# Kernel tuning notes

Hardware: AMD Instinct MI355X
Metric: run time of the kernel (lower is better)

The kernel has to match this reference:

```python
import jax, jax.numpy as jnp
import numpy as np

H = 3072           # hidden_size
I = 8192           # intermediate_size
GS = 128           # quantization group size
B, S = 2, 2048


def dequant(qw, qz, scales, group_size=GS):
    """Group-wise int4 dequant: w = (q - zero) * scale.
    qw: [out, in] int8 nibbles in [0,16); qz: [out, in//g] int8; scales: [out, in//g] f32.
    """
    zp = jnp.repeat(qz.astype(jnp.float32), group_size, axis=1)
    sc = jnp.repeat(scales, group_size, axis=1)
    return (qw.astype(jnp.float32) - zp) * sc


def setup_inputs() -> dict:
    key = jax.random.key(0)
    ks = jax.random.split(key, 8)
    hidden_states = jax.random.normal(ks[0], (B, S, H), dtype=jnp.float32)
    # gate_up projection: [2*I, H], group-quantized along the input (H) dim
    gup_qw = jax.random.randint(ks[1], (2 * I, H), 0, 16, dtype=jnp.int8)
    gup_qz = jax.random.randint(ks[2], (2 * I, H // GS), 0, 16, dtype=jnp.int8)
    gup_scales = jax.random.uniform(ks[3], (2 * I, H // GS), dtype=jnp.float32, minval=0.005, maxval=0.02)
    # down projection: [H, I], group-quantized along the input (I) dim
    down_qw = jax.random.randint(ks[4], (H, I), 0, 16, dtype=jnp.int8)
    down_qz = jax.random.randint(ks[5], (H, I // GS), 0, 16, dtype=jnp.int8)
    down_scales = jax.random.uniform(ks[6], (H, I // GS), dtype=jnp.float32, minval=0.005, maxval=0.02)
    down_bias = jnp.zeros((H,), dtype=jnp.float32)
    return {
        "hidden_states": hidden_states,
        "gup_qw": gup_qw, "gup_qz": gup_qz, "gup_scales": gup_scales,
        "down_qw": down_qw, "down_qz": down_qz, "down_scales": down_scales,
        "down_bias": down_bias,
    }


def reference(hidden_states, gup_qw, gup_qz, gup_scales, down_qw, down_qz, down_scales, down_bias):
    W_gup = dequant(gup_qw, gup_qz, gup_scales)           # [2I, H]
    up_states = jnp.einsum('bsh,oh->bso', hidden_states, W_gup)  # [B,S,2I]
    gate, up = jnp.split(up_states, 2, axis=-1)
    act = jax.nn.silu(gate) * up                          # fused gate*act*up
    W_down = dequant(down_qw, down_qz, down_scales)       # [H, I]
    out = jnp.einsum('bsi,hi->bsh', act, W_down) + down_bias
    return out
```

## Files before the change

kernel.cpp:

```cpp
#include <hip/hip_runtime.h>


typedef float f32x4 __attribute__((ext_vector_type(4)));
typedef int   i32x4 __attribute__((ext_vector_type(4)));

__device__ __forceinline__ void gload16(const void* g, void* l) {
  __builtin_amdgcn_global_load_lds(
      (const __attribute__((address_space(1))) void*)g,
      (__attribute__((address_space(3))) void*)l, 16, 0, 0);
}

__global__ __launch_bounds__(256) void quant_x(const float* __restrict__ x,
                                               signed char* __restrict__ Xq,
                                               float* __restrict__ XsT) {
  int gidx = blockIdx.x * 4 + (threadIdx.x >> 6);
  int lane = threadIdx.x & 63;
  int row = gidx / 24;
  int g   = gidx - row * 24;
  const float2 v = *(const float2*)(x + (size_t)row * 3072 + g * 128 + lane * 2);
  float m = fmaxf(fabsf(v.x), fabsf(v.y));
#pragma unroll
  for (int s = 1; s < 64; s <<= 1) m = fmaxf(m, __shfl_xor(m, s));
  float inv = m > 0.f ? 127.f / m : 0.f;
  int qa = (int)rintf(v.x * inv);
  int qb = (int)rintf(v.y * inv);
  unsigned short pk = (unsigned short)((qa & 0xff) | ((qb & 0xff) << 8));
  *(unsigned short*)(Xq + (size_t)row * 3072 + g * 128 + lane * 2) = pk;
  if (lane == 0) XsT[g * 4096 + row] = m * (1.f / 127.f);
}

template <int K>
__global__ __launch_bounds__(256) void requant_k(const int* __restrict__ qw,
                                                 const int* __restrict__ qz,
                                                 signed char* __restrict__ W) {
  constexpr int KG = K / 128;
  constexpr int perrow = K / 8;
  int idx = blockIdx.x * 256 + threadIdx.x;
  int row = idx / perrow;
  int c8  = idx - row * perrow;
  int k   = c8 << 3;
  int z   = qz[row * KG + (k >> 7)];
  const int4* q4 = (const int4*)(qw + (size_t)row * K + k);
  int4 qa = q4[0];
  int4 qb = q4[1];
  int b0 = ((qa.x - z) & 0xff) | (((qa.y - z) & 0xff) << 8) |
           (((qa.z - z) & 0xff) << 16) | (((qa.w - z) & 0xff) << 24);
  int b1 = ((qb.x - z) & 0xff) | (((qb.y - z) & 0xff) << 8) |
           (((qb.z - z) & 0xff) << 16) | (((qb.w - z) & 0xff) << 24);
  int2 o; o.x = b0; o.y = b1;
  *(int2*)(W + (size_t)row * K + k) = o;
}

__global__ __launch_bounds__(256) void transpose_sc(const float* __restrict__ in,
                                                    float* __restrict__ out,
                                                    int R, int G) {
  int idx = blockIdx.x * 256 + threadIdx.x;
  int r = idx / G;
  int g = idx - r * G;
  out[(size_t)g * R + r] = in[idx];
}


__global__ __launch_bounds__(256, 2) void gemm_gateup_i8(
    const signed char* __restrict__ Xq, const signed char* __restrict__ Wq,
    const float* __restrict__ XsT,
    const float* __restrict__ GsT,
    signed char* __restrict__ act,
    float* __restrict__ AsT) {
  const int K = 3072;
  const int bid = blockIdx.x;
  const int xcd = bid & 7;
  const int jb  = bid >> 3;
  const int n0  = ((xcd << 3) + (jb & 7)) * 128;
  const int m0  = (jb >> 3) * 128;
  __shared__ signed char lA[16384];
  __shared__ signed char lG[16384];
  __shared__ signed char lU[16384];
  __shared__ float rmax[2][128];

  const int tid  = threadIdx.x;
  const int l    = tid & 63;
  const int quad = l >> 4;
  const int l16  = l & 15;
  const int wcI  = (tid >> 6) & 1;
  const int wr   = ((tid >> 6) >> 1) * 64;
  const int wc   = wcI * 64;

  f32x4 fg[4][4] = {};
  f32x4 fu[4][4] = {};

  int off[4];
#pragma unroll
  for (int jj = 0; jj < 4; ++jj) {
    int c   = tid + 256 * jj;
    int row = c >> 3;
    int log = (c & 7) ^ (row & 7);
    off[jj] = row * K + log * 16;
  }
  const signed char* baseA = Xq + (size_t)m0 * K;
  const signed char* baseG = Wq + (size_t)n0 * K;
  const signed char* baseU = Wq + (size_t)(8192 + n0) * K;

  int aoff[2][4], boff[2][4];
#pragma unroll
  for (int h = 0; h < 2; ++h) {
    int slot = h * 4 + quad;
#pragma unroll
    for (int i = 0; i < 4; ++i) {
      int ra = wr + i * 16 + l16;
      aoff[h][i] = ra * 128 + ((slot ^ (ra & 7)) * 16);
      int rb = wc + i * 16 + l16;
      boff[h][i] = rb * 128 + ((slot ^ (rb & 7)) * 16);
    }
  }

  for (int g = 0; g < 24; ++g) {
    const int kk = g << 7;
#pragma unroll
    for (int jj = 0; jj < 4; ++jj) {
      gload16(baseA + off[jj] + kk, lA + (tid + 256 * jj) * 16);
      gload16(baseG + off[jj] + kk, lG + (tid + 256 * jj) * 16);
      gload16(baseU + off[jj] + kk, lU + (tid + 256 * jj) * 16);
    }
    f32x4 sx[4];
    float sg[4], su[4];
#pragma unroll
    for (int i = 0; i < 4; ++i)
      sx[i] = *(const f32x4*)(XsT + g * 4096 + m0 + wr + i * 16 + quad * 4);
#pragma unroll
    for (int jj = 0; jj < 4; ++jj) {
      sg[jj] = GsT[g * 16384 + n0 + wc + jj * 16 + l16];
      su[jj] = GsT[g * 16384 + 8192 + n0 + wc + jj * 16 + l16];
    }
    __syncthreads();

    i32x4 a[4][2];
#pragma unroll
    for (int i = 0; i < 4; ++i) {
      a[i][0] = *(const i32x4*)(lA + aoff[0][i]);
      a[i][1] = *(const i32x4*)(lA + aoff[1][i]);
    }
#pragma unroll
    for (int jj = 0; jj < 4; ++jj) {
      i32x4 bg0 = *(const i32x4*)(lG + boff[0][jj]);
      i32x4 bg1 = *(const i32x4*)(lG + boff[1][jj]);
      i32x4 bu0 = *(const i32x4*)(lU + boff[0][jj]);
      i32x4 bu1 = *(const i32x4*)(lU + boff[1][jj]);
#pragma unroll
      for (int i = 0; i < 4; ++i) {
        i32x4 zero = {0, 0, 0, 0};
        i32x4 ig = __builtin_amdgcn_mfma_i32_16x16x64_i8(a[i][0], bg0, zero, 0, 0, 0);
        ig = __builtin_amdgcn_mfma_i32_16x16x64_i8(a[i][1], bg1, ig, 0, 0, 0);
        i32x4 iu = __builtin_amdgcn_mfma_i32_16x16x64_i8(a[i][0], bu0, zero, 0, 0, 0);
        iu = __builtin_amdgcn_mfma_i32_16x16x64_i8(a[i][1], bu1, iu, 0, 0, 0);
#pragma unroll
        for (int r = 0; r < 4; ++r) {
          float sc = sx[i][r];
          fg[i][jj][r] = fmaf((float)ig[r], sc * sg[jj], fg[i][jj][r]);
          fu[i][jj][r] = fmaf((float)iu[r], sc * su[jj], fu[i][jj][r]);
        }
      }
    }
    __syncthreads();
  }

#pragma unroll
  for (int i = 0; i < 4; ++i)
#pragma unroll
    for (int jj = 0; jj < 4; ++jj)
#pragma unroll
      for (int r = 0; r < 4; ++r) {
        float gv = fg[i][jj][r];
        float uv = fu[i][jj][r];
        fg[i][jj][r] = (gv / (1.f + __expf(-gv))) * uv;
      }

  float rmx[4][4];
#pragma unroll
  for (int i = 0; i < 4; ++i)
#pragma unroll
    for (int r = 0; r < 4; ++r) {
      float m = 0.f;
#pragma unroll
      for (int jj = 0; jj < 4; ++jj) m = fmaxf(m, fabsf(fg[i][jj][r]));
      m = fmaxf(m, __shfl_xor(m, 1));
      m = fmaxf(m, __shfl_xor(m, 2));
      m = fmaxf(m, __shfl_xor(m, 4));
      m = fmaxf(m, __shfl_xor(m, 8));
      rmx[i][r] = m;
    }
  if (l16 == 0) {
#pragma unroll
    for (int i = 0; i < 4; ++i)
#pragma unroll
      for (int r = 0; r < 4; ++r)
        rmax[wcI][wr + i * 16 + quad * 4 + r] = rmx[i][r];
  }
  __syncthreads();

#pragma unroll
  for (int i = 0; i < 4; ++i)
#pragma unroll
    for (int r = 0; r < 4; ++r) {
      int mrow = wr + i * 16 + quad * 4 + r;
      float mx = fmaxf(rmax[0][mrow], rmax[1][mrow]);
      float inv = mx > 0.f ? 127.f / mx : 0.f;
#pragma unroll
      for (int jj = 0; jj < 4; ++jj) {
        int q = (int)rintf(fg[i][jj][r] * inv);
        lA[mrow * 128 + wc + jj * 16 + l16] = (signed char)q;
      }
    }
  if (tid < 128) {
    float mx = fmaxf(rmax[0][tid], rmax[1][tid]);
    AsT[(n0 >> 7) * 4096 + m0 + tid] = mx * (1.f / 127.f);
  }
  __syncthreads();

#pragma unroll
  for (int t = 0; t < 4; ++t) {
    int c = tid + 256 * t;
    int row = c >> 3;
    int col = (c & 7) * 16;
    *(int4*)(act + (size_t)(m0 + row) * 8192 + n0 + col) = *(const int4*)(lA + row * 128 + col);
  }
}

__global__ __launch_bounds__(256, 2) void gemm_down_i8(
    const signed char* __restrict__ Aq, const signed char* __restrict__ Wq,
    const float* __restrict__ AsT,
    const float* __restrict__ DsT,
    const float* __restrict__ bias,
    float* __restrict__ out) {
  const int K = 8192;
  const int bid = blockIdx.x;
  const int xcd = bid & 7;
  const int jb  = bid >> 3;
  const int jn  = jb % 12;
  const int jm  = jb / 12;
  const int n0  = (12 * (xcd & 1) + jn) * 128;
  const int m0  = (8 * (xcd >> 1) + jm) * 128;
  __shared__ signed char lA[16384];
  __shared__ signed char lB[16384];

  const int tid  = threadIdx.x;
  const int l    = tid & 63;
  const int quad = l >> 4;
  const int l16  = l & 15;
  const int wr   = ((tid >> 6) >> 1) * 64;
  const int wc   = ((tid >> 6) & 1) * 64;

  f32x4 fc[4][4] = {};

  int off[4];
#pragma unroll
  for (int jj = 0; jj < 4; ++jj) {
    int c   = tid + 256 * jj;
    int row = c >> 3;
    int log = (c & 7) ^ (row & 7);
    off[jj] = row * K + log * 16;
  }
  const signed char* baseA = Aq + (size_t)m0 * K;
  const signed char* baseB = Wq + (size_t)n0 * K;

  int aoff[2][4], boff[2][4];
#pragma unroll
  for (int h = 0; h < 2; ++h) {
    int slot = h * 4 + quad;
#pragma unroll
    for (int i = 0; i < 4; ++i) {
      int ra = wr + i * 16 + l16;
      aoff[h][i] = ra * 128 + ((slot ^ (ra & 7)) * 16);
      int rb = wc + i * 16 + l16;
      boff[h][i] = rb * 128 + ((slot ^ (rb & 7)) * 16);
    }
  }

  for (int g = 0; g < 64; ++g) {
    const int kk = g << 7;
#pragma unroll
    for (int jj = 0; jj < 4; ++jj) {
      gload16(baseA + off[jj] + kk, lA + (tid + 256 * jj) * 16);
      gload16(baseB + off[jj] + kk, lB + (tid + 256 * jj) * 16);
    }
    f32x4 sx[4];
    float sn[4];
#pragma unroll
    for (int i = 0; i < 4; ++i)
      sx[i] = *(const f32x4*)(AsT + g * 4096 + m0 + wr + i * 16 + quad * 4);
#pragma unroll
    for (int jj = 0; jj < 4; ++jj)
      sn[jj] = DsT[g * 3072 + n0 + wc + jj * 16 + l16];
    __syncthreads();

    i32x4 a[4][2];
#pragma unroll
    for (int i = 0; i < 4; ++i) {
      a[i][0] = *(const i32x4*)(lA + aoff[0][i]);
      a[i][1] = *(const i32x4*)(lA + aoff[1][i]);
    }
#pragma unroll
    for (int jj = 0; jj < 4; ++jj) {
      i32x4 b0 = *(const i32x4*)(lB + boff[0][jj]);
      i32x4 b1 = *(const i32x4*)(lB + boff[1][jj]);
#pragma unroll
      for (int i = 0; i < 4; ++i) {
        i32x4 zero = {0, 0, 0, 0};
        i32x4 ic = __builtin_amdgcn_mfma_i32_16x16x64_i8(a[i][0], b0, zero, 0, 0, 0);
        ic = __builtin_amdgcn_mfma_i32_16x16x64_i8(a[i][1], b1, ic, 0, 0, 0);
#pragma unroll
        for (int r = 0; r < 4; ++r)
          fc[i][jj][r] = fmaf((float)ic[r], sx[i][r] * sn[jj], fc[i][jj][r]);
      }
    }
    __syncthreads();
  }

  float bj[4];
#pragma unroll
  for (int jj = 0; jj < 4; ++jj) bj[jj] = bias[n0 + wc + jj * 16 + l16];

#pragma unroll
  for (int i = 0; i < 4; ++i)
#pragma unroll
    for (int jj = 0; jj < 4; ++jj)
#pragma unroll
      for (int r = 0; r < 4; ++r) {
        int m = m0 + wr + i * 16 + quad * 4 + r;
        int n = n0 + wc + jj * 16 + l16;
        out[(size_t)m * 3072 + n] = fc[i][jj][r] + bj[jj];
      }
}

extern "C" void kernel_launch(void* const* d_in, const int* in_sizes, int n_in,
                              void* d_out, int out_size, void* d_ws, size_t ws_size,
                              hipStream_t stream) {
  const float* x        = (const float*)d_in[0];
  const int*   gup_qw   = (const int*)d_in[1];
  const int*   gup_qz   = (const int*)d_in[2];
  const float* gup_sc   = (const float*)d_in[3];
  const int*   down_qw  = (const int*)d_in[4];
  const int*   down_qz  = (const int*)d_in[5];
  const float* down_sc  = (const float*)d_in[6];
  const float* down_b   = (const float*)d_in[7];
  float* out = (float*)d_out;

  char* ws = (char*)d_ws;
  signed char* Xq    = (signed char*)(ws);
  signed char* Wgupq = (signed char*)(ws + 12582912);
  signed char* Wdnq  = (signed char*)(ws + 62914560);
  signed char* Actq  = (signed char*)(ws + 88080384);
  float* XsT = (float*)(ws + 121634816);
  float* GsT = (float*)(ws + 122028032);
  float* DsT = (float*)(ws + 123600896);
  float* AsT = (float*)(ws + 124387328);

  quant_x<<<24576, 256, 0, stream>>>(x, Xq, XsT);
  requant_k<3072><<<24576, 256, 0, stream>>>(gup_qw, gup_qz, Wgupq);
  requant_k<8192><<<12288, 256, 0, stream>>>(down_qw, down_qz, Wdnq);
  transpose_sc<<<1536, 256, 0, stream>>>(gup_sc, GsT, 16384, 24);
  transpose_sc<<<768, 256, 0, stream>>>(down_sc, DsT, 3072, 64);
  gemm_gateup_i8<<<2048, 256, 0, stream>>>(Xq, Wgupq, XsT, GsT, Actq, AsT);
  gemm_down_i8<<<768, 256, 0, stream>>>(Actq, Wdnq, AsT, DsT, down_b, out);
}
```

Before: 837.3 us.

## Share activation quant scales across 4-row groups and use packed f32x2 FMAs

Activation quantization scales for X and for the intermediate act are now shared by groups of 4 rows instead of one per row. Inside the GEMM loops each MFMA output vector then needs a single scale product, so the dequant-accumulate can use packed 2-wide FMAs. This is meant to cut VALU work and scale loads in the inner loop of both GEMMs. In exchange, quantization is coarser (one max over 4 rows), which raises quantization error for rows with smaller magnitudes.

```diff
diff --git a/kernel.cpp b/kernel.cpp
--- a/kernel.cpp
+++ b/kernel.cpp
@@ -2,6 +2,7 @@
 
 
 typedef float f32x4 __attribute__((ext_vector_type(4)));
+typedef float f32x2 __attribute__((ext_vector_type(2)));
 typedef int   i32x4 __attribute__((ext_vector_type(4)));
 
 __device__ __forceinline__ void gload16(const void* g, void* l) {
@@ -12,21 +13,26 @@
 
 __global__ __launch_bounds__(256) void quant_x(const float* __restrict__ x,
                                                signed char* __restrict__ Xq,
-                                               float* __restrict__ XsT) {
-  int gidx = blockIdx.x * 4 + (threadIdx.x >> 6);
+                                               float* __restrict__ Xs4) {
+  int g    = blockIdx.x;
+  int rq   = blockIdx.y;
+  int w    = threadIdx.x >> 6;
   int lane = threadIdx.x & 63;
-  int row = gidx / 24;
-  int g   = gidx - row * 24;
+  int row  = rq * 4 + w;
+  __shared__ float wmax[4];
   const float2 v = *(const float2*)(x + (size_t)row * 3072 + g * 128 + lane * 2);
   float m = fmaxf(fabsf(v.x), fabsf(v.y));
 #pragma unroll
   for (int s = 1; s < 64; s <<= 1) m = fmaxf(m, __shfl_xor(m, s));
-  float inv = m > 0.f ? 127.f / m : 0.f;
+  if (lane == 0) wmax[w] = m;
+  __syncthreads();
+  float m4 = fmaxf(fmaxf(wmax[0], wmax[1]), fmaxf(wmax[2], wmax[3]));
+  float inv = m4 > 0.f ? 127.f / m4 : 0.f;
   int qa = (int)rintf(v.x * inv);
   int qb = (int)rintf(v.y * inv);
   unsigned short pk = (unsigned short)((qa & 0xff) | ((qb & 0xff) << 8));
   *(unsigned short*)(Xq + (size_t)row * 3072 + g * 128 + lane * 2) = pk;
-  if (lane == 0) XsT[g * 4096 + row] = m * (1.f / 127.f);
+  if (threadIdx.x == 0) Xs4[g * 1024 + rq] = m4 * (1.f / 127.f);
 }
 
 template <int K>
@@ -63,10 +69,10 @@
 
 __global__ __launch_bounds__(256, 2) void gemm_gateup_i8(
     const signed char* __restrict__ Xq, const signed char* __restrict__ Wq,
-    const float* __restrict__ XsT,
+    const float* __restrict__ Xs4,
     const float* __restrict__ GsT,
     signed char* __restrict__ act,
-    float* __restrict__ AsT) {
+    float* __restrict__ As4) {
   const int K = 3072;
   const int bid = blockIdx.x;
   const int xcd = bid & 7;
@@ -77,6 +83,7 @@
   __shared__ signed char lG[16384];
   __shared__ signed char lU[16384];
   __shared__ float rmax[2][128];
+  __shared__ float rmax4[32];
 
   const int tid  = threadIdx.x;
   const int l    = tid & 63;
@@ -86,8 +93,8 @@
   const int wr   = ((tid >> 6) >> 1) * 64;
   const int wc   = wcI * 64;
 
-  f32x4 fg[4][4] = {};
-  f32x4 fu[4][4] = {};
+  f32x2 fg[4][4][2] = {};
+  f32x2 fu[4][4][2] = {};
 
   int off[4];
 #pragma unroll
@@ -113,6 +120,7 @@
       boff[h][i] = rb * 128 + ((slot ^ (rb & 7)) * 16);
     }
   }
+  const int qbase = (m0 >> 2) + (wr >> 2) + quad;
 
   for (int g = 0; g < 24; ++g) {
     const int kk = g << 7;
@@ -122,11 +130,9 @@
       gload16(baseG + off[jj] + kk, lG + (tid + 256 * jj) * 16);
       gload16(baseU + off[jj] + kk, lU + (tid + 256 * jj) * 16);
     }
-    f32x4 sx[4];
-    float sg[4], su[4];
-#pragma unroll
-    for (int i = 0; i < 4; ++i)
-      sx[i] = *(const f32x4*)(XsT + g * 4096 + m0 + wr + i * 16 + quad * 4);
+    float sxq[4], sg[4], su[4];
+#pragma unroll
+    for (int i = 0; i < 4; ++i) sxq[i] = Xs4[g * 1024 + qbase + i * 4];
 #pragma unroll
     for (int jj = 0; jj < 4; ++jj) {
       sg[jj] = GsT[g * 16384 + n0 + wc + jj * 16 + l16];
@@ -153,67 +159,72 @@
         ig = __builtin_amdgcn_mfma_i32_16x16x64_i8(a[i][1], bg1, ig, 0, 0, 0);
         i32x4 iu = __builtin_amdgcn_mfma_i32_16x16x64_i8(a[i][0], bu0, zero, 0, 0, 0);
         iu = __builtin_amdgcn_mfma_i32_16x16x64_i8(a[i][1], bu1, iu, 0, 0, 0);
-#pragma unroll
-        for (int r = 0; r < 4; ++r) {
-          float sc = sx[i][r];
-          fg[i][jj][r] = fmaf((float)ig[r], sc * sg[jj], fg[i][jj][r]);
-          fu[i][jj][r] = fmaf((float)iu[r], sc * su[jj], fu[i][jj][r]);
-        }
+        float pgs = sxq[i] * sg[jj];
+        float pus = sxq[i] * su[jj];
+        f32x2 pg2 = {pgs, pgs};
+        f32x2 pu2 = {pus, pus};
+        f32x2 g01 = {(float)ig[0], (float)ig[1]};
+        f32x2 g23 = {(float)ig[2], (float)ig[3]};
+        f32x2 u01 = {(float)iu[0], (float)iu[1]};
+        f32x2 u23 = {(float)iu[2], (float)iu[3]};
+        fg[i][jj][0] = __builtin_elementwise_fma(g01, pg2, fg[i][jj][0]);
+        fg[i][jj][1] = __builtin_elementwise_fma(g23, pg2, fg[i][jj][1]);
+        fu[i][jj][0] = __builtin_elementwise_fma(u01, pu2, fu[i][jj][0]);
+        fu[i][jj][1] = __builtin_elementwise_fma(u23, pu2, fu[i][jj][1]);
       }
     }
     __syncthreads();
   }
 
+  float av[4][4][4];
 #pragma unroll
   for (int i = 0; i < 4; ++i)
 #pragma unroll
     for (int jj = 0; jj < 4; ++jj)
 #pragma unroll
       for (int r = 0; r < 4; ++r) {
-        float gv = fg[i][jj][r];
-        float uv = fu[i][jj][r];
-        fg[i][jj][r] = (gv / (1.f + __expf(-gv))) * uv;
-      }
-
-  float rmx[4][4];
+        float gv = fg[i][jj][r >> 1][r & 1];
+        float uv = fu[i][jj][r >> 1][r & 1];
+        av[i][jj][r] = (gv / (1.f + __expf(-gv))) * uv;
+      }
+
 #pragma unroll
   for (int i = 0; i < 4; ++i)
 #pragma unroll
     for (int r = 0; r < 4; ++r) {
       float m = 0.f;
 #pragma unroll
-      for (int jj = 0; jj < 4; ++jj) m = fmaxf(m, fabsf(fg[i][jj][r]));
+      for (int jj = 0; jj < 4; ++jj) m = fmaxf(m, fabsf(av[i][jj][r]));
       m = fmaxf(m, __shfl_xor(m, 1));
       m = fmaxf(m, __shfl_xor(m, 2));
       m = fmaxf(m, __shfl_xor(m, 4));
       m = fmaxf(m, __shfl_xor(m, 8));
-      rmx[i][r] = m;
-    }
-  if (l16 == 0) {
-#pragma unroll
-    for (int i = 0; i < 4; ++i)
-#pragma unroll
-      for (int r = 0; r < 4; ++r)
-        rmax[wcI][wr + i * 16 + quad * 4 + r] = rmx[i][r];
-  }
+      if (l16 == 0) rmax[wcI][wr + i * 16 + quad * 4 + r] = m;
+    }
   __syncthreads();
-
-#pragma unroll
-  for (int i = 0; i < 4; ++i)
+  if (tid < 32) {
+    float m = 0.f;
+#pragma unroll
+    for (int k = 0; k < 4; ++k)
+      m = fmaxf(m, fmaxf(rmax[0][tid * 4 + k], rmax[1][tid * 4 + k]));
+    rmax4[tid] = m;
+    As4[(n0 >> 7) * 1024 + (m0 >> 2) + tid] = m * (1.f / 127.f);
+  }
+  __syncthreads();
+
+#pragma unroll
+  for (int i = 0; i < 4; ++i) {
+    float mx = rmax4[(wr >> 2) + i * 4 + quad];
+    float inv = mx > 0.f ? 127.f / mx : 0.f;
 #pragma unroll
     for (int r = 0; r < 4; ++r) {
       int mrow = wr + i * 16 + quad * 4 + r;
-      float mx = fmaxf(rmax[0][mrow], rmax[1][mrow]);
-      float inv = mx > 0.f ? 127.f / mx : 0.f;
 #pragma unroll
       for (int jj = 0; jj < 4; ++jj) {
-        int q = (int)rintf(fg[i][jj][r] * inv);
+        int q = (int)rintf(av[i][jj][r] * inv);
         lA[mrow * 128 + wc + jj * 16 + l16] = (signed char)q;
       }
     }
-  if (tid < 128) {
-    float mx = fmaxf(rmax[0][tid], rmax[1][tid]);
-    AsT[(n0 >> 7) * 4096 + m0 + tid] = mx * (1.f / 127.f);
   }
   __syncthreads();
 
@@ -228,7 +239,7 @@
 
 __global__ __launch_bounds__(256, 2) void gemm_down_i8(
     const signed char* __restrict__ Aq, const signed char* __restrict__ Wq,
-    const float* __restrict__ AsT,
+    const float* __restrict__ As4,
     const float* __restrict__ DsT,
     const float* __restrict__ bias,
     float* __restrict__ out) {
@@ -250,7 +261,7 @@
   const int wr   = ((tid >> 6) >> 1) * 64;
   const int wc   = ((tid >> 6) & 1) * 64;
 
-  f32x4 fc[4][4] = {};
+  f32x2 fc[4][4][2] = {};
 
   int off[4];
 #pragma unroll
@@ -275,6 +286,7 @@
       boff[h][i] = rb * 128 + ((slot ^ (rb & 7)) * 16);
     }
   }
+  const int qbase = (m0 >> 2) + (wr >> 2) + quad;
 
   for (int g = 0; g < 64; ++g) {
     const int kk = g << 7;
@@ -283,11 +295,9 @@
       gload16(baseA + off[jj] + kk, lA + (tid + 256 * jj) * 16);
       gload16(baseB + off[jj] + kk, lB + (tid + 256 * jj) * 16);
     }
-    f32x4 sx[4];
-    float sn[4];
-#pragma unroll
-    for (int i = 0; i < 4; ++i)
-      sx[i] = *(const f32x4*)(AsT + g * 4096 + m0 + wr + i * 16 + quad * 4);
+    float sxq[4], sn[4];
+#pragma unroll
+    for (int i = 0; i < 4; ++i) sxq[i] = As4[g * 1024 + qbase + i * 4];
 #pragma unroll
     for (int jj = 0; jj < 4; ++jj)
       sn[jj] = DsT[g * 3072 + n0 + wc + jj * 16 + l16];
@@ -308,9 +318,12 @@
         i32x4 zero = {0, 0, 0, 0};
         i32x4 ic = __builtin_amdgcn_mfma_i32_16x16x64_i8(a[i][0], b0, zero, 0, 0, 0);
         ic = __builtin_amdgcn_mfma_i32_16x16x64_i8(a[i][1], b1, ic, 0, 0, 0);
-#pragma unroll
-        for (int r = 0; r < 4; ++r)
-          fc[i][jj][r] = fmaf((float)ic[r], sx[i][r] * sn[jj], fc[i][jj][r]);
+        float ps = sxq[i] * sn[jj];
+        f32x2 p2 = {ps, ps};
+        f32x2 c01 = {(float)ic[0], (float)ic[1]};
+        f32x2 c23 = {(float)ic[2], (float)ic[3]};
+        fc[i][jj][0] = __builtin_elementwise_fma(c01, p2, fc[i][jj][0]);
+        fc[i][jj][1] = __builtin_elementwise_fma(c23, p2, fc[i][jj][1]);
       }
     }
     __syncthreads();
@@ -328,7 +341,7 @@
       for (int r = 0; r < 4; ++r) {
         int m = m0 + wr + i * 16 + quad * 4 + r;
         int n = n0 + wc + jj * 16 + l16;
-        out[(size_t)m * 3072 + n] = fc[i][jj][r] + bj[jj];
+        out[(size_t)m * 3072 + n] = fc[i][jj][r >> 1][r & 1] + bj[jj];
       }
 }
 
@@ -350,16 +363,16 @@
   signed char* Wgupq = (signed char*)(ws + 12582912);
   signed char* Wdnq  = (signed char*)(ws + 62914560);
   signed char* Actq  = (signed char*)(ws + 88080384);
-  float* XsT = (float*)(ws + 121634816);
-  float* GsT = (float*)(ws + 122028032);
-  float* DsT = (float*)(ws + 123600896);
-  float* AsT = (float*)(ws + 124387328);
-
-  quant_x<<<24576, 256, 0, stream>>>(x, Xq, XsT);
+  float* Xs4 = (float*)(ws + 121634816);
+  float* GsT = (float*)(ws + 121733120);
+  float* DsT = (float*)(ws + 123305984);
+  float* As4 = (float*)(ws + 124092416);
+
+  quant_x<<<dim3(24, 1024), 256, 0, stream>>>(x, Xq, Xs4);
   requant_k<3072><<<24576, 256, 0, stream>>>(gup_qw, gup_qz, Wgupq);
   requant_k<8192><<<12288, 256, 0, stream>>>(down_qw, down_qz, Wdnq);
   transpose_sc<<<1536, 256, 0, stream>>>(gup_sc, GsT, 16384, 24);
   transpose_sc<<<768, 256, 0, stream>>>(down_sc, DsT, 3072, 64);
-  gemm_gateup_i8<<<2048, 256, 0, stream>>>(Xq, Wgupq, XsT, GsT, Actq, AsT);
-  gemm_down_i8<<<768, 256, 0, stream>>>(Actq, Wdnq, AsT, DsT, down_b, out);
-}
+  gemm_gateup_i8<<<2048, 256, 0, stream>>>(Xq, Wgupq, Xs4, GsT, Actq, As4);
+  gemm_down_i8<<<768, 256, 0, stream>>>(Actq, Wdnq, As4, DsT, down_b, out);
+}
```

After: 806.9 us. 1.04x faster.
